# Kernel tuning notes

Measured on AMD Instinct MI355X. Metric: run time of the kernel, lower is better.

## Reference

```python
import jax, jax.numpy as jnp
import numpy as np
import math

NUM_CLASSES = 80
CENTER_RADIUS = 2.5
EPS = 1e-7
IMG = 1280.0


def _ciou(gt, pd):
    # gt: [G,4] xyxy, pd: [A,4] xyxy -> CIoU [G,A] (matches ultralytics bbox_iou, CIoU=True)
    b1 = gt[:, None, :]
    b2 = pd[None, :, :]
    iw = jnp.clip(jnp.minimum(b1[..., 2], b2[..., 2]) - jnp.maximum(b1[..., 0], b2[..., 0]), 0.0)
    ih = jnp.clip(jnp.minimum(b1[..., 3], b2[..., 3]) - jnp.maximum(b1[..., 1], b2[..., 1]), 0.0)
    inter = iw * ih
    w1 = b1[..., 2] - b1[..., 0]; h1 = b1[..., 3] - b1[..., 1]
    w2 = b2[..., 2] - b2[..., 0]; h2 = b2[..., 3] - b2[..., 1]
    union = w1 * h1 + w2 * h2 - inter + EPS
    iou = inter / union
    cw = jnp.maximum(b1[..., 2], b2[..., 2]) - jnp.minimum(b1[..., 0], b2[..., 0])
    ch = jnp.maximum(b1[..., 3], b2[..., 3]) - jnp.minimum(b1[..., 1], b2[..., 1])
    c2 = cw * cw + ch * ch + EPS
    rho2 = ((b2[..., 0] + b2[..., 2] - b1[..., 0] - b1[..., 2]) ** 2 +
            (b2[..., 1] + b2[..., 3] - b1[..., 1] - b1[..., 3]) ** 2) / 4.0
    v = (4.0 / math.pi ** 2) * (jnp.arctan(w2 / (h2 + EPS)) - jnp.arctan(w1 / (h1 + EPS))) ** 2
    alpha = v / (v - iou + (1.0 + EPS))
    return iou - (rho2 / c2 + v * alpha)


def _assign_one(scores, boxes, gt_lab, gt_box, valid, stride, anc):
    # scores [A,C], boxes [A,4], gt_lab [G], gt_box [G,4], valid [G] bool, stride [A,1], anc [A,2]
    G = gt_lab.shape[0]
    C = scores.shape[-1]
    # geometry constraint: anchor center within radius*stride of gt center
    gcx = (gt_box[:, 0] + gt_box[:, 2]) / 2.0
    gcy = (gt_box[:, 1] + gt_box[:, 3]) / 2.0
    cd = (stride[:, 0] * CENTER_RADIUS)[None, :]            # [1,A]
    in_center = (jnp.abs(anc[None, :, 0] - gcx[:, None]) < cd) & \
                (jnp.abs(anc[None, :, 1] - gcy[:, None]) < cd)
    in_center = in_center & valid[:, None]                  # [G,A]
    anchor_filter = in_center.any(axis=0)                   # [A]
    # pairwise CIoU (zeroed outside the filtered anchor set / invalid gts)
    ious = jnp.clip(_ciou(gt_box, boxes), 0.0)
    ious = ious * anchor_filter[None, :].astype(ious.dtype) * valid[:, None].astype(ious.dtype)
    iou_loss = -jnp.log(ious + 1e-8)
    # BCE(sqrt(p), onehot) summed over classes, computed without [G,A,C] tensor:
    # sum_c BCE = -sum_c log(1-p_c) - log p_{c_g} + log(1-p_{c_g})
    p = jnp.sqrt(scores)
    logp = jnp.clip(jnp.log(p), -100.0)
    log1mp = jnp.clip(jnp.log1p(-p), -100.0)
    base = -log1mp.sum(-1)                                  # [A]
    lp_g = jnp.take(logp, gt_lab, axis=1).T                 # [G,A]
    l1m_g = jnp.take(log1mp, gt_lab, axis=1).T              # [G,A]
    cls_loss = base[None, :] - lp_g + l1m_g
    # cost; extra 1e8/1e9 penalties emulate torch's exclusion of unfiltered anchors / invalid gts
    cost = (cls_loss + 3.0 * iou_loss
            + 1e6 * (~in_center).astype(cls_loss.dtype)
            + 1e8 * (~anchor_filter)[None, :].astype(cls_loss.dtype)
            + 1e9 * (~valid)[:, None].astype(cls_loss.dtype))
    # dynamic-k: sum of top-10 ious per gt
    topk_ious = jax.lax.top_k(ious, 10)[0]
    dyn_k = jnp.maximum((topk_ious.sum(-1) + 0.5).astype(jnp.int32), 1)
    # per-gt pick dyn_k lowest-cost anchors via rank
    ranks = jnp.argsort(jnp.argsort(cost, axis=-1), axis=-1)
    matching = (ranks < dyn_k[:, None]) & valid[:, None]    # [G,A] bool
    # conflict resolution: anchors matched to >1 gt keep min-cost gt
    cnt = matching.sum(0)                                   # [A]
    best_g = jnp.argmin(cost, axis=0)                       # [A]
    onehot_g = jnp.arange(G)[:, None] == best_g[None, :]
    matching = jnp.where(cnt[None, :] > 1, onehot_g, matching)
    fg = matching.any(axis=0)                               # [A]
    mg = jnp.argmax(matching, axis=0)                       # [A]
    pred_iou = (matching.astype(ious.dtype) * ious).sum(0)  # [A]
    labels = jnp.where(fg, gt_lab[mg], NUM_CLASSES).astype(jnp.int32)
    tboxes = gt_box[mg] * fg[:, None].astype(gt_box.dtype)
    tscores = jax.nn.one_hot(gt_lab[mg], C, dtype=scores.dtype) * (pred_iou * fg)[:, None]
    tgt_idx = jnp.where(fg, mg, 0).astype(jnp.int32)
    return labels, tboxes, tscores, fg, tgt_idx


def setup_inputs() -> dict:
    key = jax.random.key(0)
    ks = jax.random.split(key, 10)
    bs, A, G, C = 16, 33600, 64, NUM_CLASSES
    pd_scores = jax.random.uniform(ks[0], (bs, A, C), jnp.float32, 1e-4, 0.99)
    cxy = jax.random.uniform(ks[1], (bs, A, 2), jnp.float32, 0.0, IMG)
    wh = jax.random.uniform(ks[2], (bs, A, 2), jnp.float32, 8.0, 128.0)
    pd_bboxes = jnp.concatenate([cxy - wh / 2, cxy + wh / 2], axis=-1)
    anc_points = jax.random.uniform(ks[3], (A, 2), jnp.float32, 0.0, IMG)
    gt_labels = jax.random.randint(ks[4], (bs, G, 1), 0, C, jnp.int32)
    gcxy = jax.random.uniform(ks[5], (bs, G, 2), jnp.float32, 64.0, IMG - 64.0)
    gwh = jax.random.uniform(ks[6], (bs, G, 2), jnp.float32, 16.0, 256.0)
    gt_bboxes = jnp.concatenate([gcxy - gwh / 2, gcxy + gwh / 2], axis=-1)
    mask_gt = (jax.random.randint(ks[7], (bs, G, 1), 0, 5, jnp.int32) < 4).astype(jnp.int32)
    stride = (8.0 * (2.0 ** jax.random.randint(ks[8], (bs, A, 1), 0, 3, jnp.int32).astype(jnp.float32)))
    return {"pd_scores": pd_scores, "pd_bboxes": pd_bboxes, "anc_points": anc_points,
            "gt_labels": gt_labels, "gt_bboxes": gt_bboxes, "mask_gt": mask_gt, "stride": stride}


def reference(pd_scores, pd_bboxes, anc_points, gt_labels, gt_bboxes, mask_gt, stride):
    gt_lab = gt_labels[..., 0].astype(jnp.int32)
    valid = mask_gt[..., 0].astype(bool)
    fn = jax.vmap(_assign_one, in_axes=(0, 0, 0, 0, 0, 0, None))
    return fn(pd_scores, pd_bboxes, gt_lab, gt_bboxes, valid, stride, anc_points)
```

## Files before the change

### kernel.cpp

```cpp
#include <hip/hip_runtime.h>
#include <float.h>
#include <math.h>

#define NA 33600
#define NG 64
#define NC 80
#define NB 16
#define CRAD 2.5f
#define MCAP 12288

typedef float vfloat4 __attribute__((ext_vector_type(4)));

#define O_CNT   0ULL
#define O_AG    2150400ULL
#define O_AIOU  4300800ULL
#define O_BASE  6451200ULL
#define O_CCNT  8601600ULL
#define O_CONFC 8601664ULL
#define O_CONFL 8601728ULL
#define O_CA    8667264ULL
#define O_CBASE 9453696ULL
#define O_COLT  10240128ULL
#define WS_NEED_COLT (10240128ULL + 62914560ULL)
#define O_CPB   73154688ULL
#define O_CAP   76300416ULL
#define WS_NEED_PC (76300416ULL + 3145728ULL)

#define OFF_LAB 0L
#define OFF_TB  537600L
#define OFF_TS  2688000L
#define OFF_FG  45696000L
#define OFF_TGT 46233600L
#define OUT_TOTAL 46771200L

__device__ __forceinline__ float ciou_clip(float gx1, float gy1, float gx2, float gy2,
                                           float w1, float h1, float at1, float at2v,
                                           float4 pb) {
    float iw = fmaxf(fminf(gx2, pb.z) - fmaxf(gx1, pb.x), 0.f);
    float ih = fmaxf(fminf(gy2, pb.w) - fmaxf(gy1, pb.y), 0.f);
    float inter = iw * ih;
    float w2 = pb.z - pb.x, h2 = pb.w - pb.y;
    float uni = w1 * h1 + w2 * h2 - inter + 1e-7f;
    float iou = inter / uni;
    float cw = fmaxf(gx2, pb.z) - fminf(gx1, pb.x);
    float ch = fmaxf(gy2, pb.w) - fminf(gy1, pb.y);
    float c2 = cw * cw + ch * ch + 1e-7f;
    float dx = pb.x + pb.z - gx1 - gx2;
    float dy = pb.y + pb.w - gy1 - gy2;
    float rho2 = (dx * dx + dy * dy) * 0.25f;
    float dat = at2v - at1;
    float v = 0.4052847345693511f * (dat * dat);
    float alpha = v / ((v - iou) + 1.0000001f);
    float ci = iou - (rho2 / c2 + v * alpha);
    return fmaxf(ci, 0.f);
}

__global__ __launch_bounds__(256) void k1a_cand(
    const float* __restrict__ anc, const float* __restrict__ gbox,
    const int* __restrict__ gmask, const float* __restrict__ strd,
    int* __restrict__ candA, int* __restrict__ candCnt, int* __restrict__ cnt)
{
    __shared__ float s_gcx[NG], s_gcy[NG];
    __shared__ int s_val[NG];
    const int b = blockIdx.y, tid = threadIdx.x;
    if (tid < NG) {
        const float4 gb = ((const float4*)gbox)[b * NG + tid];
        s_gcx[tid] = (gb.x + gb.z) * 0.5f;
        s_gcy[tid] = (gb.y + gb.w) * 0.5f;
        s_val[tid] = gmask[b * NG + tid];
    }
    __syncthreads();
    const int a = blockIdx.x * 256 + tid;
    int f = 0;
    if (a < NA) {
        cnt[(long)b * NA + a] = 0;
        float2 ap = ((const float2*)anc)[a];
        float cd = strd[(long)b * NA + a] * CRAD;
        for (int g = 0; g < NG; ++g)
            if (s_val[g] && fabsf(ap.x - s_gcx[g]) < cd && fabsf(ap.y - s_gcy[g]) < cd) { f = 1; break; }
    }
    unsigned long long m = __ballot(f);
    int lane = tid & 63;
    int wcnt = __popcll(m);
    int pre = __popcll(m & ((1ULL << lane) - 1ULL));
    int base0 = 0;
    if (lane == 0 && wcnt) base0 = atomicAdd(&candCnt[b], wcnt);
    base0 = __shfl(base0, 0, 64);
    if (f) {
        int pos = base0 + pre;
        if (pos < MCAP) candA[b * MCAP + pos] = a;
    }
}

__global__ __launch_bounds__(256) void k1b_gather(
    const float* __restrict__ scores, const float* __restrict__ pdb,
    const float* __restrict__ anc, const float* __restrict__ strd,
    const int* __restrict__ candCnt, const int* __restrict__ candA,
    float* __restrict__ base, float* __restrict__ candBase,
    float* __restrict__ colT, int use_colT,
    float4* __restrict__ candPB, float4* __restrict__ candAp, int use_pc)
{
    __shared__ float s_l1m[64][81];
    const int b = blockIdx.y;
    int M = candCnt[b]; if (M > MCAP) M = MCAP;
    if (blockIdx.x * 64 >= M) return;
    const int q   = threadIdx.x >> 2;
    const int sub = threadIdx.x & 3;
    const int j = blockIdx.x * 64 + q;
    const bool active = (j < M);
    int a = 0;
    if (active) a = candA[b * MCAP + j];
    const long ia = (long)b * NA + a;
    if (active) {
        if (sub == 1 && use_pc) {
            float4 pb = ((const float4*)pdb)[ia];
            float2 ap = ((const float2*)anc)[a];
            float cd = strd[ia] * CRAD;
            float at2v = atanf((pb.z - pb.x) / ((pb.w - pb.y) + 1e-7f));
            candPB[b * MCAP + j] = pb;
            candAp[b * MCAP + j] = make_float4(ap.x, ap.y, cd, at2v);
        }
        const vfloat4* srow = (const vfloat4*)(scores + ia * NC);
        float* ct = colT + (long)b * NC * MCAP + j;
        #pragma unroll
        for (int qq = 0; qq < 5; ++qq) {
            vfloat4 s4 = __builtin_nontemporal_load(&srow[sub * 5 + qq]);
            float sv[4] = {s4.x, s4.y, s4.z, s4.w};
            #pragma unroll
            for (int k = 0; k < 4; ++k) {
                const int c = sub * 20 + 4 * qq + k;
                float p = sqrtf(sv[k]);
                float l1m = fmaxf(log1pf(-p), -100.f);
                s_l1m[q][c] = l1m;
                if (use_colT) {
                    float lp = fmaxf(logf(p), -100.f);
                    __builtin_nontemporal_store(l1m - lp, &ct[(long)c * MCAP]);
                }
            }
        }
    }
    __syncthreads();
    if (active && sub == 0) {
        float bsum = 0.f;
        #pragma unroll
        for (int c = 0; c < NC; ++c)
            bsum += s_l1m[q][c];
        const float bval = -bsum;
        base[ia] = bval;
        candBase[b * MCAP + j] = bval;
    }
}

__global__ __launch_bounds__(512) void k2_select(
    const float* __restrict__ scores, const float* __restrict__ pdb,
    const float* __restrict__ anc, const int* __restrict__ glab,
    const float* __restrict__ gbox, const int* __restrict__ gmask,
    const float* __restrict__ strd,
    const int* __restrict__ candCnt, const int* __restrict__ candA,
    const float* __restrict__ candBase, const float* __restrict__ colT, int use_colT,
    const float4* __restrict__ candPB, const float4* __restrict__ candAp, int use_pc,
    int* __restrict__ cnt, int* __restrict__ ag, float* __restrict__ aiou)
{
    const int i = blockIdx.x;
    const int b = (i & 7) | ((i >> 9) << 3);
    const int g = (i >> 3) & 63;
    if (gmask[b * NG + g] == 0) return;
    const int tid = threadIdx.x, lane = tid & 63, wid = tid >> 6;
    __shared__ float s_v[8];
    __shared__ int s_i[8];

    const float4 gb = ((const float4*)gbox)[b * NG + g];
    const int lab = glab[b * NG + g];
    const float gcx = (gb.x + gb.z) * 0.5f, gcy = (gb.y + gb.w) * 0.5f;
    const float w1 = gb.z - gb.x, h1 = gb.w - gb.y;
    const float at1 = atanf(w1 / (h1 + 1e-7f));
    const long bA = (long)b * NA;
    const int bM = b * MCAP;
    int M = candCnt[b]; if (M > MCAP) M = MCAP;
    const float* colrow = colT + (long)(b * NC + lab) * MCAP;

    float liou[10]; int liodx[10];
    float lcost[10]; int lidx[10]; float lci[10];
    #pragma unroll
    for (int j = 0; j < 10; ++j) {
        liou[j] = 0.f;  liodx[j] = 0x40000000 + tid * 10 + j;
        lcost[j] = FLT_MAX; lidx[j] = 0x40000000 + tid * 10 + j; lci[j] = 0.f;
    }

    for (int jj = tid; jj < M; jj += 512) {
        const int a = candA[bM + jj];
        const long ia = bA + a;
        float4 pb; float apx, apy, cd, at2v;
        if (use_pc) {
            pb = candPB[bM + jj];
            float4 t = candAp[bM + jj];
            apx = t.x; apy = t.y; cd = t.z; at2v = t.w;
        } else {
            pb = ((const float4*)pdb)[ia];
            at2v = atanf((pb.z - pb.x) / ((pb.w - pb.y) + 1e-7f));
            float2 ap = ((const float2*)anc)[a];
            apx = ap.x; apy = ap.y;
            cd = strd[ia] * CRAD;
        }
        float ci = ciou_clip(gb.x, gb.y, gb.z, gb.w, w1, h1, at1, at2v, pb);
        bool inc = (fabsf(apx - gcx) < cd) && (fabsf(apy - gcy) < cd);
        float colv;
        if (use_colT) {
            colv = candBase[bM + jj] + colrow[jj];
        } else {
            float s = scores[ia * (long)NC + lab];
            float p = sqrtf(s);
            colv = candBase[bM + jj] + (fmaxf(log1pf(-p), -100.f) - fmaxf(logf(p), -100.f));
        }
        float cost = colv + 3.0f * (-logf(ci + 1e-8f));
        if (!inc) cost += 1e6f;

        if (ci > 0.f && (ci > liou[9] || (ci == liou[9] && a < liodx[9]))) {
            int p10 = 0;
            #pragma unroll
            for (int k = 0; k < 10; ++k)
                p10 += (liou[k] > ci || (liou[k] == ci && liodx[k] < a)) ? 1 : 0;
            #pragma unroll
            for (int j = 9; j >= 0; --j) {
                float pv = (j > 0) ? liou[j - 1] : 0.f;
                int pvi  = (j > 0) ? liodx[j - 1] : 0;
                bool sh = (j > p10), he = (j == p10);
                liou[j]  = sh ? pv  : (he ? ci : liou[j]);
                liodx[j] = sh ? pvi : (he ? a  : liodx[j]);
            }
        }
        if (cost < lcost[9] || (cost == lcost[9] && a < lidx[9])) {
            int p10 = 0;
            #pragma unroll
            for (int k = 0; k < 10; ++k)
                p10 += (lcost[k] < cost || (lcost[k] == cost && lidx[k] < a)) ? 1 : 0;
            #pragma unroll
            for (int j = 9; j >= 0; --j) {
                float pv = (j > 0) ? lcost[j - 1] : FLT_MAX;
                int pvi  = (j > 0) ? lidx[j - 1] : 0;
                float pvc = (j > 0) ? lci[j - 1] : 0.f;
                bool sh = (j > p10), he = (j == p10);
                lcost[j] = sh ? pv  : (he ? cost : lcost[j]);
                lidx[j]  = sh ? pvi : (he ? a    : lidx[j]);
                lci[j]   = sh ? pvc : (he ? ci   : lci[j]);
            }
        }
    }

    float acc = 0.f;
    for (int it = 0; it < 10; ++it) {
        float bv = -2.f; int bi = 0x7fffffff;
        #pragma unroll
        for (int j = 0; j < 10; ++j)
            if (liou[j] > bv || (liou[j] == bv && liodx[j] < bi)) { bv = liou[j]; bi = liodx[j]; }
        for (int off = 32; off > 0; off >>= 1) {
            float ov = __shfl_down(bv, off, 64);
            int   oi = __shfl_down(bi, off, 64);
            if (ov > bv || (ov == bv && oi < bi)) { bv = ov; bi = oi; }
        }
        if (lane == 0) { s_v[wid] = bv; s_i[wid] = bi; }
        __syncthreads();
        float wv = s_v[0]; int wi = s_i[0];
        #pragma unroll
        for (int w = 1; w < 8; ++w)
            if (s_v[w] > wv || (s_v[w] == wv && s_i[w] < wi)) { wv = s_v[w]; wi = s_i[w]; }
        acc += wv;
        #pragma unroll
        for (int j = 0; j < 10; ++j)
            if (liou[j] == wv && liodx[j] == wi) { liou[j] = -2.f; liodx[j] = 0x7fffffff; }
        __syncthreads();
    }
    int K = (int)(acc + 0.5f);
    if (K < 1) K = 1;

    for (int it = 0; it < K; ++it) {
        float bc = FLT_MAX; int bi = 0x7fffffff;
        #pragma unroll
        for (int j = 0; j < 10; ++j)
            if (lcost[j] < bc || (lcost[j] == bc && lidx[j] < bi)) { bc = lcost[j]; bi = lidx[j]; }
        for (int off = 32; off > 0; off >>= 1) {
            float oc = __shfl_down(bc, off, 64);
            int   oi = __shfl_down(bi, off, 64);
            if (oc < bc || (oc == bc && oi < bi)) { bc = oc; bi = oi; }
        }
        if (lane == 0) { s_v[wid] = bc; s_i[wid] = bi; }
        __syncthreads();
        float wc = s_v[0]; int wi = s_i[0];
        #pragma unroll
        for (int w = 1; w < 8; ++w)
            if (s_v[w] < wc || (s_v[w] == wc && s_i[w] < wi)) { wc = s_v[w]; wi = s_i[w]; }
        if (wi < NA) {
            #pragma unroll
            for (int j = 0; j < 10; ++j)
                if (lcost[j] == wc && lidx[j] == wi) {
                    atomicAdd(&cnt[bA + wi], 1);
                    ag[bA + wi] = g;
                    aiou[bA + wi] = lci[j];
                    lcost[j] = FLT_MAX; lidx[j] = 0x7fffffff;
                }
        }
        __syncthreads();
    }
}

__global__ __launch_bounds__(256) void k3_main(
    const int* __restrict__ glab, const float* __restrict__ gbox,
    const int* __restrict__ cnt, const int* __restrict__ ag, const float* __restrict__ aiou,
    int* __restrict__ confCnt, int* __restrict__ confList, float* __restrict__ out)
{
    const int tid = threadIdx.x;
    const long i = (long)blockIdx.x * 256 + tid;
    const int b = (int)(i / NA);
    const int c = cnt[i];
    float labo = 80.f;
    const bool conflict = (c > 1);
    if (c == 1) {
        int g = ag[i]; float iou = aiou[i];
        int lb = glab[b * NG + g];
        labo = (float)lb;
        ((float4*)(out + OFF_TB))[i] = ((const float4*)gbox)[b * NG + g];
        out[OFF_FG + i] = 1.f;
        out[OFF_TGT + i] = (float)g;
        out[OFF_TS + i * NC + lb] = iou;
    }
    unsigned long long m = __ballot(conflict ? 1 : 0);
    int lane = tid & 63;
    int wcnt = __popcll(m);
    int pre = __popcll(m & ((1ULL << lane) - 1ULL));
    int base0 = 0;
    if (lane == 0 && wcnt) base0 = atomicAdd(confCnt, wcnt);
    base0 = __shfl(base0, 0, 64);
    if (conflict) confList[base0 + pre] = (int)i;
    else out[OFF_LAB + i] = labo;
}

__global__ __launch_bounds__(256) void k3b_conflict(
    const float* __restrict__ scores, const float* __restrict__ pdb,
    const float* __restrict__ anc, const int* __restrict__ glab,
    const float* __restrict__ gbox, const int* __restrict__ gmask,
    const float* __restrict__ strd, const float* __restrict__ base,
    const int* __restrict__ confCnt, const int* __restrict__ confList,
    float* __restrict__ out)
{
    const int lane = threadIdx.x & 63;
    const int waveId = blockIdx.x * 4 + (threadIdx.x >> 6);
    const int nWaves = gridDim.x * 4;
    int n = *confCnt; if (n > 16384) n = 16384;
    for (int idx = waveId; idx < n; idx += nWaves) {
        const long i = (long)confList[idx];
        const int b = (int)(i / NA); const int a = (int)(i % NA);
        const int g = lane;
        float4 pb = ((const float4*)pdb)[i];
        float bse = base[i];
        float at2v = atanf((pb.z - pb.x) / ((pb.w - pb.y) + 1e-7f));
        float2 ap = ((const float2*)anc)[a];
        float cd = strd[i] * CRAD;
        float cost = FLT_MAX; float iom = 0.f;
        if (gmask[b * NG + g] != 0) {
            float4 gb = ((const float4*)gbox)[b * NG + g];
            float w1 = gb.z - gb.x, h1 = gb.w - gb.y;
            float at1 = atanf(w1 / (h1 + 1e-7f));
            iom = ciou_clip(gb.x, gb.y, gb.z, gb.w, w1, h1, at1, at2v, pb);
            float gcx = (gb.x + gb.z) * 0.5f, gcy = (gb.y + gb.w) * 0.5f;
            bool inc = (fabsf(ap.x - gcx) < cd) && (fabsf(ap.y - gcy) < cd);
            int lb = glab[b * NG + g];
            float s = scores[i * (long)NC + lb];
            float p = sqrtf(s);
            float clsv = bse + (fmaxf(log1pf(-p), -100.f) - fmaxf(logf(p), -100.f));
            cost = clsv + 3.0f * (-logf(iom + 1e-8f));
            if (!inc) cost += 1e6f;
        }
        float bc = cost; int bg = g; float bio = iom;
        for (int off = 32; off > 0; off >>= 1) {
            float oc = __shfl_down(bc, off, 64);
            int   og = __shfl_down(bg, off, 64);
            float oo = __shfl_down(bio, off, 64);
            if (oc < bc || (oc == bc && og < bg)) { bc = oc; bg = og; bio = oo; }
        }
        if (lane == 0) {
            int lb = glab[b * NG + bg];
            out[OFF_LAB + i] = (float)lb;
            ((float4*)(out + OFF_TB))[i] = ((const float4*)gbox)[b * NG + bg];
            out[OFF_FG + i] = 1.f;
            out[OFF_TGT + i] = (float)bg;
            out[OFF_TS + i * NC + lb] = bio;
        }
    }
}

extern "C" void kernel_launch(void* const* d_in, const int* in_sizes, int n_in,
                              void* d_out, int out_size, void* d_ws, size_t ws_size,
                              hipStream_t stream) {
    const float* scores = (const float*)d_in[0];
    const float* pdb    = (const float*)d_in[1];
    const float* anc    = (const float*)d_in[2];
    const int*   glab   = (const int*)d_in[3];
    const float* gbox   = (const float*)d_in[4];
    const int*   gmask  = (const int*)d_in[5];
    const float* strd   = (const float*)d_in[6];
    float* out = (float*)d_out;
    char* ws = (char*)d_ws;

    int*    cnt      = (int*)(ws + O_CNT);
    int*    ag       = (int*)(ws + O_AG);
    float*  aiou     = (float*)(ws + O_AIOU);
    float*  base     = (float*)(ws + O_BASE);
    int*    candCnt  = (int*)(ws + O_CCNT);
    int*    confCnt  = (int*)(ws + O_CONFC);
    int*    confList = (int*)(ws + O_CONFL);
    int*    candA    = (int*)(ws + O_CA);
    float*  candBase = (float*)(ws + O_CBASE);
    float*  colT     = (float*)(ws + O_COLT);
    float4* candPB   = (float4*)(ws + O_CPB);
    float4* candAp   = (float4*)(ws + O_CAP);
    const int use_colT = (ws_size >= WS_NEED_COLT) ? 1 : 0;
    const int use_pc   = (ws_size >= WS_NEED_PC) ? 1 : 0;

    (void)hipMemsetAsync(out + OFF_TB, 0, (size_t)(OUT_TOTAL - OFF_TB) * sizeof(float), stream);
    (void)hipMemsetAsync(candCnt, 0, 128, stream);
    k1a_cand<<<dim3((NA + 255) / 256, NB), 256, 0, stream>>>(
        anc, gbox, gmask, strd, candA, candCnt, cnt);
    k1b_gather<<<dim3((MCAP + 63) / 64, NB), 256, 0, stream>>>(
        scores, pdb, anc, strd, candCnt, candA, base, candBase, colT, use_colT,
        candPB, candAp, use_pc);
    k2_select<<<NB * NG, 512, 0, stream>>>(
        scores, pdb, anc, glab, gbox, gmask, strd,
        candCnt, candA, candBase, colT, use_colT, candPB, candAp, use_pc,
        cnt, ag, aiou);
    k3_main<<<(NB * NA) / 256, 256, 0, stream>>>(
        glab, gbox, cnt, ag, aiou, confCnt, confList, out);
    k3b_conflict<<<128, 256, 0, stream>>>(
        scores, pdb, anc, glab, gbox, gmask, strd, base,
        confCnt, confList, out);
}
```

Baseline: 611.9 us.

## Split per-GT top-k selection into two-block scan plus wave-level merge

The per-(batch,gt) selection kernel is split into a scan kernel in which two 256-thread blocks each cover half of the candidates and write their local top-10 IoU and top-10 cost lists to workspace. A separate merge kernel then uses one wavefront per gt to combine the 20 partial entries, compute the dynamic K, and scatter the assignments. The aim is more parallelism and shorter serial block-wide reductions, at the cost of an extra kernel launch and a round trip through workspace. The fallback select kernel is resized to 256 threads.

```diff
diff --git a/kernel.cpp b/kernel.cpp
--- a/kernel.cpp
+++ b/kernel.cpp
@@ -25,6 +25,11 @@
 #define O_CPB   73154688ULL
 #define O_CAP   76300416ULL
 #define WS_NEED_PC (76300416ULL + 3145728ULL)
+#define O_PIOU  79446144ULL
+#define O_PCST  79528064ULL
+#define O_PIDX  79609984ULL
+#define O_PCI   79691904ULL
+#define WS_NEED_SPLIT 79773824ULL
 
 #define OFF_LAB 0L
 #define OFF_TB  537600L
@@ -151,7 +156,187 @@
     }
 }
 
-__global__ __launch_bounds__(512) void k2_select(
+__global__ __launch_bounds__(256) void k2_scan(
+    const int* __restrict__ glab, const float* __restrict__ gbox,
+    const int* __restrict__ gmask,
+    const int* __restrict__ candCnt, const int* __restrict__ candA,
+    const float* __restrict__ candBase, const float* __restrict__ colT,
+    const float4* __restrict__ candPB, const float4* __restrict__ candAp,
+    float* __restrict__ partIou, float* __restrict__ partCost,
+    int* __restrict__ partIdx, float* __restrict__ partCi)
+{
+    const int i = blockIdx.y;
+    const int s = blockIdx.x;
+    const int b = (i & 7) | ((i >> 9) << 3);
+    const int g = (i >> 3) & 63;
+    if (gmask[b * NG + g] == 0) return;
+    const int tid = threadIdx.x, lane = tid & 63, wid = tid >> 6;
+    __shared__ float s_v[4];
+    __shared__ int s_i[4];
+
+    const float4 gb = ((const float4*)gbox)[b * NG + g];
+    const int lab = glab[b * NG + g];
+    const float gcx = (gb.x + gb.z) * 0.5f, gcy = (gb.y + gb.w) * 0.5f;
+    const float w1 = gb.z - gb.x, h1 = gb.w - gb.y;
+    const float at1 = atanf(w1 / (h1 + 1e-7f));
+    const int bM = b * MCAP;
+    int M = candCnt[b]; if (M > MCAP) M = MCAP;
+    const float* colrow = colT + (long)(b * NC + lab) * MCAP;
+
+    float liou[10]; int liodx[10];
+    float lcost[10]; int lidx[10]; float lci[10];
+    #pragma unroll
+    for (int j = 0; j < 10; ++j) {
+        liou[j] = 0.f;  liodx[j] = 0x40000000 + tid * 10 + j;
+        lcost[j] = FLT_MAX; lidx[j] = 0x40000000 + tid * 10 + j; lci[j] = 0.f;
+    }
+
+    for (int jj = s * 256 + tid; jj < M; jj += 512) {
+        const int a = candA[bM + jj];
+        float4 pb = candPB[bM + jj];
+        float4 t  = candAp[bM + jj];
+        float ci = ciou_clip(gb.x, gb.y, gb.z, gb.w, w1, h1, at1, t.w, pb);
+        bool inc = (fabsf(t.x - gcx) < t.z) && (fabsf(t.y - gcy) < t.z);
+        float colv = candBase[bM + jj] + colrow[jj];
+        float cost = colv + 3.0f * (-logf(ci + 1e-8f));
+        if (!inc) cost += 1e6f;
+
+        if (ci > 0.f && (ci > liou[9] || (ci == liou[9] && a < liodx[9]))) {
+            int p10 = 0;
+            #pragma unroll
+            for (int k = 0; k < 10; ++k)
+                p10 += (liou[k] > ci || (liou[k] == ci && liodx[k] < a)) ? 1 : 0;
+            #pragma unroll
+            for (int j = 9; j >= 0; --j) {
+                float pv = (j > 0) ? liou[j - 1] : 0.f;
+                int pvi  = (j > 0) ? liodx[j - 1] : 0;
+                bool sh = (j > p10), he = (j == p10);
+                liou[j]  = sh ? pv  : (he ? ci : liou[j]);
+                liodx[j] = sh ? pvi : (he ? a  : liodx[j]);
+            }
+        }
+        if (cost < lcost[9] || (cost == lcost[9] && a < lidx[9])) {
+            int p10 = 0;
+            #pragma unroll
+            for (int k = 0; k < 10; ++k)
+                p10 += (lcost[k] < cost || (lcost[k] == cost && lidx[k] < a)) ? 1 : 0;
+            #pragma unroll
+            for (int j = 9; j >= 0; --j) {
+                float pv = (j > 0) ? lcost[j - 1] : FLT_MAX;
+                int pvi  = (j > 0) ? lidx[j - 1] : 0;
+                float pvc = (j > 0) ? lci[j - 1] : 0.f;
+                bool sh = (j > p10), he = (j == p10);
+                lcost[j] = sh ? pv  : (he ? cost : lcost[j]);
+                lidx[j]  = sh ? pvi : (he ? a    : lidx[j]);
+                lci[j]   = sh ? pvc : (he ? ci   : lci[j]);
+            }
+        }
+    }
+
+    const int pbase = i * 20 + s * 10;
+    for (int it = 0; it < 10; ++it) {
+        float bv = -2.f; int bi = 0x7fffffff;
+        #pragma unroll
+        for (int j = 0; j < 10; ++j)
+            if (liou[j] > bv || (liou[j] == bv && liodx[j] < bi)) { bv = liou[j]; bi = liodx[j]; }
+        for (int off = 32; off > 0; off >>= 1) {
+            float ov = __shfl_down(bv, off, 64);
+            int   oi = __shfl_down(bi, off, 64);
+            if (ov > bv || (ov == bv && oi < bi)) { bv = ov; bi = oi; }
+        }
+        if (lane == 0) { s_v[wid] = bv; s_i[wid] = bi; }
+        __syncthreads();
+        float wv = s_v[0]; int wi = s_i[0];
+        #pragma unroll
+        for (int w = 1; w < 4; ++w)
+            if (s_v[w] > wv || (s_v[w] == wv && s_i[w] < wi)) { wv = s_v[w]; wi = s_i[w]; }
+        if (tid == 0) partIou[pbase + it] = wv;
+        #pragma unroll
+        for (int j = 0; j < 10; ++j)
+            if (liou[j] == wv && liodx[j] == wi) { liou[j] = -2.f; liodx[j] = 0x7fffffff; }
+        __syncthreads();
+    }
+    for (int it = 0; it < 10; ++it) {
+        float bc = FLT_MAX; int bi = 0x7fffffff;
+        #pragma unroll
+        for (int j = 0; j < 10; ++j)
+            if (lcost[j] < bc || (lcost[j] == bc && lidx[j] < bi)) { bc = lcost[j]; bi = lidx[j]; }
+        for (int off = 32; off > 0; off >>= 1) {
+            float oc = __shfl_down(bc, off, 64);
+            int   oi = __shfl_down(bi, off, 64);
+            if (oc < bc || (oc == bc && oi < bi)) { bc = oc; bi = oi; }
+        }
+        if (lane == 0) { s_v[wid] = bc; s_i[wid] = bi; }
+        __syncthreads();
+        float wc = s_v[0]; int wi = s_i[0];
+        #pragma unroll
+        for (int w = 1; w < 4; ++w)
+            if (s_v[w] < wc || (s_v[w] == wc && s_i[w] < wi)) { wc = s_v[w]; wi = s_i[w]; }
+        #pragma unroll
+        for (int j = 0; j < 10; ++j)
+            if (lcost[j] == wc && lidx[j] == wi) {
+                partCost[pbase + it] = wc;
+                partIdx[pbase + it]  = wi;
+                partCi[pbase + it]   = lci[j];
+                lcost[j] = FLT_MAX; lidx[j] = 0x7fffffff;
+            }
+        __syncthreads();
+    }
+}
+
+__global__ __launch_bounds__(256) void k2b_merge(
+    const int* __restrict__ gmask,
+    const float* __restrict__ partIou, const float* __restrict__ partCost,
+    const int* __restrict__ partIdx, const float* __restrict__ partCi,
+    int* __restrict__ cnt, int* __restrict__ ag, float* __restrict__ aiou)
+{
+    const int lane = threadIdx.x & 63;
+    const int wv0 = blockIdx.x * 4 + (threadIdx.x >> 6);
+    for (int i = wv0; i < NB * NG; i += gridDim.x * 4) {
+        const int b = (i & 7) | ((i >> 9) << 3);
+        const int g = (i >> 3) & 63;
+        if (gmask[b * NG + g] == 0) continue;
+        float v = (lane < 20) ? partIou[i * 20 + lane] : -2.f;
+        float acc = 0.f;
+        for (int it = 0; it < 10; ++it) {
+            float bv = v;
+            for (int off = 32; off > 0; off >>= 1) {
+                float ov = __shfl_down(bv, off, 64);
+                if (ov > bv) bv = ov;
+            }
+            bv = __shfl(bv, 0, 64);
+            acc += bv;
+            unsigned long long m = __ballot(v == bv);
+            int first = (int)(__ffsll((long long)m)) - 1;
+            if (lane == first) v = -3.f;
+        }
+        int K = (int)(acc + 0.5f);
+        if (K < 1) K = 1;
+
+        float c  = (lane < 20) ? partCost[i * 20 + lane] : FLT_MAX;
+        int  idx = (lane < 20) ? partIdx[i * 20 + lane] : 0x7fffffff;
+        float ci = (lane < 20) ? partCi[i * 20 + lane] : 0.f;
+        const long bA = (long)b * NA;
+        for (int it = 0; it < K; ++it) {
+            float bc = c; int bi = idx;
+            for (int off = 32; off > 0; off >>= 1) {
+                float oc = __shfl_down(bc, off, 64);
+                int   oi = __shfl_down(bi, off, 64);
+                if (oc < bc || (oc == bc && oi < bi)) { bc = oc; bi = oi; }
+            }
+            bc = __shfl(bc, 0, 64); bi = __shfl(bi, 0, 64);
+            const bool own = (c == bc && idx == bi);
+            if (own && bi < NA) {
+                atomicAdd(&cnt[bA + bi], 1);
+                ag[bA + bi] = g;
+                aiou[bA + bi] = ci;
+            }
+            if (own) { c = FLT_MAX; idx = 0x7fffffff; }
+        }
+    }
+}
+
+__global__ __launch_bounds__(256) void k2_select(
     const float* __restrict__ scores, const float* __restrict__ pdb,
     const float* __restrict__ anc, const int* __restrict__ glab,
     const float* __restrict__ gbox, const int* __restrict__ gmask,
@@ -166,8 +351,8 @@
     const int g = (i >> 3) & 63;
     if (gmask[b * NG + g] == 0) return;
     const int tid = threadIdx.x, lane = tid & 63, wid = tid >> 6;
-    __shared__ float s_v[8];
-    __shared__ int s_i[8];
+    __shared__ float s_v[4];
+    __shared__ int s_i[4];
 
     const float4 gb = ((const float4*)gbox)[b * NG + g];
     const int lab = glab[b * NG + g];
@@ -187,7 +372,7 @@
         lcost[j] = FLT_MAX; lidx[j] = 0x40000000 + tid * 10 + j; lci[j] = 0.f;
     }
 
-    for (int jj = tid; jj < M; jj += 512) {
+    for (int jj = tid; jj < M; jj += 256) {
         const int a = candA[bM + jj];
         const long ia = bA + a;
         float4 pb; float apx, apy, cd, at2v;
@@ -262,7 +447,7 @@
         __syncthreads();
         float wv = s_v[0]; int wi = s_i[0];
         #pragma unroll
-        for (int w = 1; w < 8; ++w)
+        for (int w = 1; w < 4; ++w)
             if (s_v[w] > wv || (s_v[w] == wv && s_i[w] < wi)) { wv = s_v[w]; wi = s_i[w]; }
         acc += wv;
         #pragma unroll
@@ -287,7 +472,7 @@
         __syncthreads();
         float wc = s_v[0]; int wi = s_i[0];
         #pragma unroll
-        for (int w = 1; w < 8; ++w)
+        for (int w = 1; w < 4; ++w)
             if (s_v[w] < wc || (s_v[w] == wc && s_i[w] < wi)) { wc = s_v[w]; wi = s_i[w]; }
         if (wi < NA) {
             #pragma unroll
@@ -413,8 +598,13 @@
     float*  colT     = (float*)(ws + O_COLT);
     float4* candPB   = (float4*)(ws + O_CPB);
     float4* candAp   = (float4*)(ws + O_CAP);
-    const int use_colT = (ws_size >= WS_NEED_COLT) ? 1 : 0;
-    const int use_pc   = (ws_size >= WS_NEED_PC) ? 1 : 0;
+    float*  partIou  = (float*)(ws + O_PIOU);
+    float*  partCost = (float*)(ws + O_PCST);
+    int*    partIdx  = (int*)(ws + O_PIDX);
+    float*  partCi   = (float*)(ws + O_PCI);
+    const int use_colT  = (ws_size >= WS_NEED_COLT) ? 1 : 0;
+    const int use_pc    = (ws_size >= WS_NEED_PC) ? 1 : 0;
+    const int use_split = (ws_size >= WS_NEED_SPLIT) ? 1 : 0;
 
     (void)hipMemsetAsync(out + OFF_TB, 0, (size_t)(OUT_TOTAL - OFF_TB) * sizeof(float), stream);
     (void)hipMemsetAsync(candCnt, 0, 128, stream);
@@ -423,10 +613,18 @@
     k1b_gather<<<dim3((MCAP + 63) / 64, NB), 256, 0, stream>>>(
         scores, pdb, anc, strd, candCnt, candA, base, candBase, colT, use_colT,
         candPB, candAp, use_pc);
-    k2_select<<<NB * NG, 512, 0, stream>>>(
-        scores, pdb, anc, glab, gbox, gmask, strd,
-        candCnt, candA, candBase, colT, use_colT, candPB, candAp, use_pc,
-        cnt, ag, aiou);
+    if (use_split) {
+        k2_scan<<<dim3(2, NB * NG), 256, 0, stream>>>(
+            glab, gbox, gmask, candCnt, candA, candBase, colT, candPB, candAp,
+            partIou, partCost, partIdx, partCi);
+        k2b_merge<<<64, 256, 0, stream>>>(
+            gmask, partIou, partCost, partIdx, partCi, cnt, ag, aiou);
+    } else {
+        k2_select<<<NB * NG, 256, 0, stream>>>(
+            scores, pdb, anc, glab, gbox, gmask, strd,
+            candCnt, candA, candBase, colT, use_colT, candPB, candAp, use_pc,
+            cnt, ag, aiou);
+    }
     k3_main<<<(NB * NA) / 256, 256, 0, stream>>>(
         glab, gbox, cnt, ag, aiou, confCnt, confList, out);
     k3b_conflict<<<128, 256, 0, stream>>>(
```

After: 626.2 us. 1.02x slower.
